# Performance work log

Hardware: AMD Instinct MI355X
Metric: run time of the kernel (lower is better)

Reference implementation:

```python
import jax, jax.numpy as jnp
import numpy as np

B, C, S = 32, 64, 112
RATIO = 8
EPS = 1e-5


def conv1x1(x, w, b):
    # 1x1 conv == channel-mixing matmul. x:[B,C,H,W], w:[O,C], b:[O]
    return jnp.einsum('oc,bchw->bohw', w, x) + b[None, :, None, None]


def dwconv(x, w, b):
    # grouped 1x1 conv with groups=C: per-channel scale + bias
    return x * w[None, :, None, None] + b[None, :, None, None]


def bn(x, g, b):
    # BatchNorm2d in training mode: batch stats over (N,H,W), biased var
    m = x.mean((0, 2, 3), keepdims=True)
    v = x.var((0, 2, 3), keepdims=True)
    return (x - m) * jax.lax.rsqrt(v + EPS) * g[None, :, None, None] + b[None, :, None, None]


def avgpool(x, k):
    # nn.AvgPool2d(k): kernel k, stride k, VALID (floor) padding
    s = jax.lax.reduce_window(x, 0.0, jax.lax.add, (1, 1, k, k), (1, 1, k, k), 'VALID')
    return s / float(k * k)


def setup_inputs() -> dict:
    key = jax.random.key(0)
    ks = jax.random.split(key, 20)
    C2, H = 2 * C, (2 * C) // RATIO

    def n(k, shape, s=0.02):
        return jax.random.normal(k, shape, jnp.float32) * s

    return {
        'rgb': jax.random.normal(ks[0], (B, C, S, S), jnp.float32),
        'fre': jax.random.normal(ks[1], (B, C, S, S), jnp.float32),
        'wq_fad': n(ks[2], (C, C)), 'bq_fad': jnp.zeros((C,), jnp.float32),
        'wq_lfs': n(ks[3], (C, C)), 'bq_lfs': jnp.zeros((C,), jnp.float32),
        'wk_fad': n(ks[4], (C, C)), 'bk_fad': jnp.zeros((C,), jnp.float32),
        'wk_lfs': n(ks[5], (C, C)), 'bk_lfs': jnp.zeros((C,), jnp.float32),
        'fad_gamma': n(ks[6], (1,), 1.0), 'lfs_gamma': n(ks[7], (1,), 1.0),
        'fad_cw': n(ks[8], (C,), 1.0), 'fad_cb': jnp.zeros((C,), jnp.float32),
        'fad_bg': jnp.ones((C,), jnp.float32), 'fad_bb': jnp.zeros((C,), jnp.float32),
        'lfs_cw': n(ks[9], (C,), 1.0), 'lfs_cb': jnp.zeros((C,), jnp.float32),
        'lfs_bg': jnp.ones((C,), jnp.float32), 'lfs_bb': jnp.zeros((C,), jnp.float32),
        'lin1_w': n(ks[10], (3,), 0.3), 'lin2_w': n(ks[11], (3,), 0.3),
        'mlp_w1': n(ks[12], (H, C2)), 'mlp_w2': n(ks[13], (C2, H)),
        'rgb_cw': n(ks[14], (C,), 1.0), 'rgb_cb': jnp.zeros((C,), jnp.float32),
        'rgb_bg': jnp.ones((C,), jnp.float32), 'rgb_bb': jnp.zeros((C,), jnp.float32),
        'fre_cw': n(ks[15], (C,), 1.0), 'fre_cb': jnp.zeros((C,), jnp.float32),
        'fre_bg': jnp.ones((C,), jnp.float32), 'fre_bb': jnp.zeros((C,), jnp.float32),
    }


def reference(rgb, fre, wq_fad, bq_fad, wq_lfs, bq_lfs, wk_fad, bk_fad, wk_lfs, bk_lfs,
              fad_gamma, lfs_gamma, fad_cw, fad_cb, fad_bg, fad_bb,
              lfs_cw, lfs_cb, lfs_bg, lfs_bb, lin1_w, lin2_w, mlp_w1, mlp_w2,
              rgb_cw, rgb_cb, rgb_bg, rgb_bb, fre_cw, fre_cb, fre_bg, fre_bb):
    Bn, Cn, Sz, _ = rgb.shape
    # ---- MixBlock: cross attention over folded (B*C) batch ----
    qF = conv1x1(rgb, wq_fad, bq_fad).reshape(Bn * Cn, Sz, Sz)
    qL = conv1x1(fre, wq_lfs, bq_lfs).reshape(Bn * Cn, Sz, Sz)
    Mq = jnp.concatenate([qF, qL], axis=2)          # [BC, S, 2S]
    kF = conv1x1(rgb, wk_fad, bk_fad).reshape(Bn * Cn, Sz, Sz).transpose(0, 2, 1)
    kL = conv1x1(fre, wk_lfs, bk_lfs).reshape(Bn * Cn, Sz, Sz).transpose(0, 2, 1)
    Mk = jnp.concatenate([kF, kL], axis=1)          # [BC, 2S, S]
    attn = jax.nn.softmax(jnp.matmul(Mq, Mk), axis=-1).reshape(Bn, Cn, Sz, Sz)
    att_lfs = fre * attn * (jax.nn.sigmoid(lfs_gamma) * 2.0 - 1.0)
    y_fad = rgb + bn(dwconv(att_lfs, fad_cw, fad_cb), fad_bg, fad_bb)
    att_fad = rgb * attn * (jax.nn.sigmoid(fad_gamma) * 2.0 - 1.0)
    y_lfs = fre + bn(dwconv(att_fad, lfs_cw, lfs_cb), lfs_bg, lfs_bb)
    # ---- MSCA on concatenated channels ----
    x = jnp.concatenate([y_fad, y_lfs], axis=1)     # [B, 2C, S, S]
    avgs, maxs = [], []
    for k in (3, 5, 7):
        m = avgpool(x, k)
        avgs.append(m.mean((2, 3)))
        maxs.append(m.max((2, 3)))
    a_p = jnp.stack(avgs, -1) @ lin1_w              # [B, 2C]
    m_p = jnp.stack(maxs, -1) @ lin2_w

    def mlp(v):
        h = jax.nn.relu(jnp.einsum('rc,bc->br', mlp_w1, v))
        return jnp.einsum('cr,br->bc', mlp_w2, h)

    ca = jax.nn.sigmoid(mlp(a_p) + mlp(m_p))        # [B, 2C]
    r_c = ca[:, :Cn, None, None]
    f_c = ca[:, Cn:, None, None]
    rgb_out = y_fad + bn(dwconv(r_c * y_fad, rgb_cw, rgb_cb), rgb_bg, rgb_bb)
    fre_out = y_lfs + bn(dwconv(f_c * y_lfs, fre_cw, fre_cb), fre_bg, fre_bb)
    return (rgb_out, fre_out)
```

## Files before the change

### kernel.cpp

```cpp
#include <hip/hip_runtime.h>
#include <hip/hip_bf16.h>
#include <stdint.h>

#define NE 25690112ull
#define PP 12544
#define SS 112
#define EPSV 1e-5f

typedef __attribute__((ext_vector_type(8))) short short8v;
typedef __attribute__((ext_vector_type(4))) float float4v;

__device__ __forceinline__ unsigned short f2bf(float x){
  union { float f; uint32_t u; } v; v.f = x;
  uint32_t r = (v.u + 0x7fffu + ((v.u >> 16) & 1u)) >> 16;
  return (unsigned short)r;
}
__device__ __forceinline__ float bf2f(unsigned short u){ return __uint_as_float(((uint32_t)u) << 16); }

__global__ __launch_bounds__(256) void k1_conv(
    const float* __restrict__ rgb, const float* __restrict__ fre,
    const float* __restrict__ wq_fad, const float* __restrict__ bq_fad,
    const float* __restrict__ wk_fad, const float* __restrict__ bk_fad,
    const float* __restrict__ wq_lfs, const float* __restrict__ bq_lfs,
    const float* __restrict__ wk_lfs, const float* __restrict__ bk_lfs,
    unsigned short* __restrict__ qF, unsigned short* __restrict__ kF,
    unsigned short* __restrict__ qL, unsigned short* __restrict__ kL,
    unsigned short* __restrict__ rgbb, unsigned short* __restrict__ freb)
{
  const int bx = blockIdx.x, b = blockIdx.y, z = blockIdx.z;
  const float* X  = z ? fre : rgb;
  const float* Wq = z ? wq_lfs : wq_fad;
  const float* Bq = z ? bq_lfs : bq_fad;
  const float* Wk = z ? wk_lfs : wk_fad;
  const float* Bk = z ? bk_lfs : bk_fad;
  unsigned short* Oq = z ? qL : qF;
  unsigned short* Ok = z ? kL : kF;
  unsigned short* Xb = z ? freb : rgbb;

  __shared__ __align__(16) unsigned short xs[64 * 260];

  const int tid = threadIdx.x, lane = tid & 63, w = tid >> 6;
  const int lc = lane & 15, l4 = lane >> 4;

  const int p0 = bx*256;
  const size_t xbase = (size_t)b * 64 * PP;
  #pragma unroll
  for (int i = 0; i < 16; ++i){
    const int c = w*16 + i;
    const size_t gof = xbase + (size_t)c*PP + p0 + lane*4;
    float4 xv = *(const float4*)(X + gof);
    ushort4 s;
    s.x = f2bf(xv.x); s.y = f2bf(xv.y); s.z = f2bf(xv.z); s.w = f2bf(xv.w);
    *(ushort4*)(Xb + gof) = s;
    *(ushort4*)(&xs[c*260 + lane*4]) = s;
  }
  __syncthreads();

  short8v afr[4][2];
  #pragma unroll
  for (int t = 0; t < 4; ++t){
    const int p = (t*4 + w)*16 + lc;
    #pragma unroll
    for (int ks = 0; ks < 2; ++ks){
      short8v a;
      #pragma unroll
      for (int j = 0; j < 8; ++j)
        a[j] = (short)xs[(ks*32 + l4*8 + j)*260 + p];
      afr[t][ks] = a;
    }
  }
  __syncthreads();

  #pragma unroll
  for (int arr = 0; arr < 2; ++arr){
    const float* W = arr ? Wk : Wq;
    const float* Bi = arr ? Bk : Bq;
    unsigned short* O = arr ? Ok : Oq;
    short8v wf[4][2];
    float bias[4];
    #pragma unroll
    for (int ot = 0; ot < 4; ++ot){
      bias[ot] = Bi[ot*16 + lc];
      #pragma unroll
      for (int ks = 0; ks < 2; ++ks){
        const int base = (ot*16 + lc)*64 + ks*32 + l4*8;
        const float4 q0 = *(const float4*)(W + base);
        const float4 q1 = *(const float4*)(W + base + 4);
        short8v v;
        v[0]=(short)f2bf(q0.x); v[1]=(short)f2bf(q0.y); v[2]=(short)f2bf(q0.z); v[3]=(short)f2bf(q0.w);
        v[4]=(short)f2bf(q1.x); v[5]=(short)f2bf(q1.y); v[6]=(short)f2bf(q1.z); v[7]=(short)f2bf(q1.w);
        wf[ot][ks] = v;
      }
    }
    #pragma unroll
    for (int t = 0; t < 4; ++t){
      const int pt = (t*4 + w)*16;
      #pragma unroll
      for (int ot = 0; ot < 4; ++ot){
        float4v acc = (float4v){bias[ot], bias[ot], bias[ot], bias[ot]};
        acc = __builtin_amdgcn_mfma_f32_16x16x32_bf16(afr[t][0], wf[ot][0], acc, 0, 0, 0);
        acc = __builtin_amdgcn_mfma_f32_16x16x32_bf16(afr[t][1], wf[ot][1], acc, 0, 0, 0);
        ushort4 u;
        u.x = f2bf(acc[0]); u.y = f2bf(acc[1]); u.z = f2bf(acc[2]); u.w = f2bf(acc[3]);
        const int o = ot*16 + lc;
        uint32_t byteS = (uint32_t)(o*512 + (pt + l4*4)*2) ^ (uint32_t)((o & 7) << 4);
        *(ushort4*)((char*)xs + byteS) = u;
      }
    }
    __syncthreads();
    for (int i = tid; i < 2048; i += 256){
      const int o = i >> 5, s = i & 31;
      uint32_t byteS = (uint32_t)(o*512 + s*16) ^ (uint32_t)((o & 7) << 4);
      short8v v = *(const short8v*)((const char*)xs + byteS);
      *(short8v*)(O + ((size_t)b*64 + o)*PP + p0 + s*8) = v;
    }
    __syncthreads();
  }
}

__global__ __launch_bounds__(448) void k2_attn(
    unsigned short* __restrict__ qF, const unsigned short* __restrict__ qL,
    const unsigned short* __restrict__ kF, const unsigned short* __restrict__ kL,
    const unsigned short* __restrict__ rgbb, const unsigned short* __restrict__ freb,
    const float* __restrict__ fad_gamma, const float* __restrict__ lfs_gamma,
    float* __restrict__ stats)
{
  const int bc = blockIdx.x, c = bc & 63;
  const size_t plane = (size_t)bc * PP;
  __shared__ __align__(16) unsigned short ksF[PP + 16];
  __shared__ __align__(16) unsigned short ksL[PP + 16];
  const int tid = threadIdx.x, lane = tid & 63, w = tid >> 6;
  const int l4 = lane >> 4, lc = lane & 15;

  const unsigned short* qFp = qF + plane;
  const unsigned short* qLp = qL + plane;
  const int qrow = w*16 + lc;
  short8v aF[4], aL[4];
  #pragma unroll
  for (int ks = 0; ks < 4; ++ks){
    const int joff = ks*32 + l4*8;
    if ((ks < 3) || (l4 < 2)){
      aF[ks] = *(const short8v*)(qFp + qrow*SS + joff);
      aL[ks] = *(const short8v*)(qLp + qrow*SS + joff);
    } else {
      aF[ks] = (short8v)(short)0;
      aL[ks] = (short8v)(short)0;
    }
  }

  const uint32_t* kFu = (const uint32_t*)kF + plane/2;
  const uint32_t* kLu = (const uint32_t*)kL + plane/2;
  uint32_t* ksFw = (uint32_t*)ksF;
  uint32_t* ksLw = (uint32_t*)ksL;
  #pragma unroll
  for (int t = 0; t < 14; ++t){
    const int i = tid + t*448;
    ksFw[i] = kFu[i];
    ksLw[i] = kLu[i];
  }
  __syncthreads();

  float4v acc[7];
  #pragma unroll
  for (int ct = 0; ct < 7; ++ct) acc[ct] = (float4v)0.f;
  #pragma unroll
  for (int ks = 0; ks < 4; ++ks){
    #pragma unroll
    for (int ct = 0; ct < 7; ++ct){
      const uint32_t off = (uint32_t)((ct*16 + lc)*224 + ks*64 + l4*16);
      short8v bF = *(const short8v*)((const char*)ksF + off);
      short8v bL = *(const short8v*)((const char*)ksL + off);
      acc[ct] = __builtin_amdgcn_mfma_f32_16x16x32_bf16(aF[ks], bF, acc[ct], 0, 0, 0);
      acc[ct] = __builtin_amdgcn_mfma_f32_16x16x32_bf16(aL[ks], bL, acc[ct], 0, 0, 0);
    }
  }

  ushort4 frv[7], rgv[7];
  #pragma unroll
  for (int t = 0; t < 7; ++t){
    const int i4 = tid + t*448;
    frv[t] = *(const ushort4*)(freb + plane + (size_t)i4*4);
    rgv[t] = *(const ushort4*)(rgbb + plane + (size_t)i4*4);
  }

  const float sF = 2.f/(1.f + __expf(-fad_gamma[0])) - 1.f;
  const float sL = 2.f/(1.f + __expf(-lfs_gamma[0])) - 1.f;
  unsigned short* attnP = qF + plane;
  unsigned short* alin = ksF;

  __syncthreads();
  #pragma unroll
  for (int r = 0; r < 4; ++r){
    const int i = w*16 + l4*4 + r;
    float v[7];
    #pragma unroll
    for (int ct = 0; ct < 7; ++ct) v[ct] = acc[ct][r];
    float m = fmaxf(fmaxf(fmaxf(v[0],v[1]),fmaxf(v[2],v[3])), fmaxf(fmaxf(v[4],v[5]),v[6]));
    #pragma unroll
    for (int off = 8; off; off >>= 1) m = fmaxf(m, __shfl_xor(m, off, 64));
    float e[7]; float s = 0.f;
    #pragma unroll
    for (int ct = 0; ct < 7; ++ct){ e[ct] = __expf(v[ct] - m); s += e[ct]; }
    #pragma unroll
    for (int off = 8; off; off >>= 1) s += __shfl_xor(s, off, 64);
    const float inv = 1.f / s;
    #pragma unroll
    for (int ct = 0; ct < 7; ++ct)
      alin[i*SS + ct*16 + lc] = f2bf(e[ct] * inv);
  }
  __syncthreads();

  float ls1 = 0.f, lq1 = 0.f, ls2 = 0.f, lq2 = 0.f;
  #pragma unroll
  for (int t = 0; t < 7; ++t){
    const int i4 = tid + t*448;
    ushort4 av = *(const ushort4*)(alin + i4*4);
    *(ushort4*)(attnP + (size_t)i4*4) = av;
    const unsigned short* ap = &av.x;
    const unsigned short* fp = &frv[t].x;
    const unsigned short* rp = &rgv[t].x;
    #pragma unroll
    for (int j = 0; j < 4; ++j){
      float a = bf2f(ap[j]);
      float v1 = bf2f(fp[j]) * a * sL;
      float v2 = bf2f(rp[j]) * a * sF;
      ls1 += v1; lq1 += v1*v1; ls2 += v2; lq2 += v2*v2;
    }
  }
  #pragma unroll
  for (int off = 32; off; off >>= 1){
    ls1 += __shfl_xor(ls1, off, 64);
    lq1 += __shfl_xor(lq1, off, 64);
    ls2 += __shfl_xor(ls2, off, 64);
    lq2 += __shfl_xor(lq2, off, 64);
  }
  if (lane == 0){
    atomicAdd(&stats[c],       ls1);
    atomicAdd(&stats[64 + c],  lq1);
    atomicAdd(&stats[128 + c], ls2);
    atomicAdd(&stats[192 + c], lq2);
  }
}

__global__ void k3_affine1(const float* __restrict__ stats,
    const float* __restrict__ fad_cw, const float* __restrict__ fad_bg, const float* __restrict__ fad_bb,
    const float* __restrict__ lfs_cw, const float* __restrict__ lfs_bg, const float* __restrict__ lfs_bb,
    float* __restrict__ AB)
{
  int c = threadIdx.x;
  if (c >= 64) return;
  const float n = 401408.f;
  {
    float m1 = stats[c]/n, v1 = stats[64+c]/n - (stats[c]/n)*(stats[c]/n);
    float cw = fad_cw[c], g = fad_bg[c];
    float rs = rsqrtf(cw*cw*v1 + EPSV);
    AB[c]      = cw*rs*g;
    AB[64 + c] = -cw*m1*rs*g + fad_bb[c];
  }
  {
    float m2 = stats[128+c]/n, v2 = stats[192+c]/n - (stats[128+c]/n)*(stats[128+c]/n);
    float cw = lfs_cw[c], g = lfs_bg[c];
    float rs = rsqrtf(cw*cw*v2 + EPSV);
    AB[128 + c] = cw*rs*g;
    AB[192 + c] = -cw*m2*rs*g + lfs_bb[c];
  }
}

__global__ __launch_bounds__(512) void k4_fuse(
    const unsigned short* __restrict__ attn,
    const unsigned short* __restrict__ rgbb, const unsigned short* __restrict__ freb,
    const float* __restrict__ AB1,
    const float* __restrict__ fad_gamma, const float* __restrict__ lfs_gamma,
    unsigned short* __restrict__ ybf, unsigned short* __restrict__ ybl,
    float* __restrict__ avgstat, float* __restrict__ maxstat,
    float4* __restrict__ planeStats)
{
  const int bc = blockIdx.x, b = bc >> 6, c = bc & 63;
  const size_t plane = (size_t)bc * PP;
  __shared__ unsigned short ys[2][112][113];
  __shared__ float redA[8][4];
  __shared__ float redS[8], redM[8];
  const int tid = threadIdx.x, lane = tid & 63, w = tid >> 6;
  const float sF = 2.f/(1.f + __expf(-fad_gamma[0])) - 1.f;
  const float sL = 2.f/(1.f + __expf(-lfs_gamma[0])) - 1.f;
  const float A1 = AB1[c], B1 = AB1[64+c], A2 = AB1[128+c], B2 = AB1[192+c];
  float s0 = 0.f, q0 = 0.f, s1 = 0.f, q1 = 0.f;

  for (int i4 = tid; i4 < 3136; i4 += 512){
    ushort4 av = *(const ushort4*)(attn + plane + (size_t)i4*4);
    ushort4 rg = *(const ushort4*)(rgbb + plane + (size_t)i4*4);
    ushort4 fr = *(const ushort4*)(freb + plane + (size_t)i4*4);
    float aa[4] = {bf2f(av.x), bf2f(av.y), bf2f(av.z), bf2f(av.w)};
    float rr[4] = {bf2f(rg.x), bf2f(rg.y), bf2f(rg.z), bf2f(rg.w)};
    float ff[4] = {bf2f(fr.x), bf2f(fr.y), bf2f(fr.z), bf2f(fr.w)};
    float y0[4], y1[4];
    ushort4 o0, o1;
    unsigned short* p0 = &o0.x; unsigned short* p1 = &o1.x;
    #pragma unroll
    for (int j = 0; j < 4; ++j){
      float t1 = ff[j]*aa[j]*sL;
      float t2 = rr[j]*aa[j]*sF;
      y0[j] = rr[j] + A1*t1 + B1;
      y1[j] = ff[j] + A2*t2 + B2;
      s0 += y0[j]; q0 += y0[j]*y0[j];
      s1 += y1[j]; q1 += y1[j]*y1[j];
      p0[j] = f2bf(y0[j]);
      p1[j] = f2bf(y1[j]);
    }
    *(ushort4*)(ybf + plane + (size_t)i4*4) = o0;
    *(ushort4*)(ybl + plane + (size_t)i4*4) = o1;
    int r = i4 / 28, c0 = (i4 % 28) * 4;
    #pragma unroll
    for (int j = 0; j < 4; ++j){
      ys[0][r][c0+j] = p0[j];
      ys[1][r][c0+j] = p1[j];
    }
  }
  #pragma unroll
  for (int off = 32; off; off >>= 1){
    s0 += __shfl_xor(s0, off, 64); q0 += __shfl_xor(q0, off, 64);
    s1 += __shfl_xor(s1, off, 64); q1 += __shfl_xor(q1, off, 64);
  }
  if (lane == 0){ redA[w][0] = s0; redA[w][1] = q0; redA[w][2] = s1; redA[w][3] = q1; }
  __syncthreads();
  if (tid == 0){
    float a0=0,a1=0,a2=0,a3=0;
    for (int i = 0; i < 8; ++i){ a0+=redA[i][0]; a1+=redA[i][1]; a2+=redA[i][2]; a3+=redA[i][3]; }
    float4 ps = {a0,a1,a2,a3};
    planeStats[bc] = ps;
  }
  __syncthreads();

  const int kk[3] = {3,5,7};
  const int gg[3] = {37,22,16};
  for (int pl = 0; pl < 2; ++pl){
    const int cc = pl*64 + c;
    for (int ki = 0; ki < 3; ++ki){
      const int k = kk[ki], g = gg[ki];
      float sumAll = 0.f, mx = -3.0e38f;
      for (int win = tid; win < g*g; win += 512){
        int wy = win / g, wx = win % g;
        float s = 0.f;
        for (int dy = 0; dy < k; ++dy)
          for (int dx = 0; dx < k; ++dx)
            s += bf2f(ys[pl][wy*k+dy][wx*k+dx]);
        sumAll += s; mx = fmaxf(mx, s);
      }
      #pragma unroll
      for (int off = 32; off; off >>= 1){
        sumAll += __shfl_xor(sumAll, off, 64);
        mx = fmaxf(mx, __shfl_xor(mx, off, 64));
      }
      if (lane == 0){ redS[w] = sumAll; redM[w] = mx; }
      __syncthreads();
      if (tid == 0){
        float st = 0.f, mt = -3.0e38f;
        for (int i = 0; i < 8; ++i){ st += redS[i]; mt = fmaxf(mt, redM[i]); }
        int idx = (b*128 + cc)*3 + ki;
        avgstat[idx] = st / (float)(k*k*g*g);
        maxstat[idx] = mt / (float)(k*k);
      }
      __syncthreads();
    }
  }
}

__global__ void k6_mlp(const float* __restrict__ avgstat, const float* __restrict__ maxstat,
    const float* __restrict__ lin1, const float* __restrict__ lin2,
    const float* __restrict__ w1, const float* __restrict__ w2,
    float* __restrict__ ca)
{
  const int b = blockIdx.x, tid = threadIdx.x;
  __shared__ float sa[128], sm[128], hA[16], hM[16];
  int idx = (b*128 + tid)*3;
  sa[tid] = avgstat[idx]*lin1[0] + avgstat[idx+1]*lin1[1] + avgstat[idx+2]*lin1[2];
  sm[tid] = maxstat[idx]*lin2[0] + maxstat[idx+1]*lin2[1] + maxstat[idx+2]*lin2[2];
  __syncthreads();
  if (tid < 16){
    float ha = 0.f, hm = 0.f;
    for (int c2 = 0; c2 < 128; ++c2){
      ha += w1[tid*128 + c2]*sa[c2];
      hm += w1[tid*128 + c2]*sm[c2];
    }
    hA[tid] = fmaxf(ha, 0.f); hM[tid] = fmaxf(hm, 0.f);
  }
  __syncthreads();
  float o = 0.f;
  for (int r = 0; r < 16; ++r) o += w2[tid*16 + r]*(hA[r] + hM[r]);
  ca[b*128 + tid] = 1.f/(1.f + __expf(-o));
}

__global__ void k8_affineF(const float4* __restrict__ planeStats, const float* __restrict__ ca,
    const float* __restrict__ rgb_cw, const float* __restrict__ rgb_bg, const float* __restrict__ rgb_bb,
    const float* __restrict__ fre_cw, const float* __restrict__ fre_bg, const float* __restrict__ fre_bb,
    float* __restrict__ ABF)
{
  int t = threadIdx.x;
  if (t >= 128) return;
  int z = t >> 6, c = t & 63;
  float S = 0.f, Q = 0.f;
  for (int b = 0; b < 32; ++b){
    float4 ps = planeStats[b*64 + c];
    float sc = ca[b*128 + t];
    float sp = z ? ps.z : ps.x;
    float qp = z ? ps.w : ps.y;
    S += sc*sp; Q += sc*sc*qp;
  }
  const float n = 401408.f;
  float m = S/n, v = Q/n - m*m;
  float cw = z ? fre_cw[c] : rgb_cw[c];
  float g  = z ? fre_bg[c] : rgb_bg[c];
  float bb = z ? fre_bb[c] : rgb_bb[c];
  float rs = rsqrtf(cw*cw*v + EPSV);
  ABF[z*128 + c]      = cw*rs*g;
  ABF[z*128 + 64 + c] = -cw*m*rs*g + bb;
}

__global__ __launch_bounds__(256) void k9_out(
    const unsigned short* __restrict__ ybf, const unsigned short* __restrict__ ybl,
    const float* __restrict__ ca, const float* __restrict__ ABF,
    float* __restrict__ out)
{
  const int c = blockIdx.x, b = blockIdx.y, z = blockIdx.z;
  const size_t plane = ((size_t)b*64 + c)*PP;
  const unsigned short* y = z ? ybl : ybf;
  float* o = out + (z ? NE : 0) + plane;
  const float sc = ca[b*128 + z*64 + c];
  const float A = ABF[z*128 + c], Bv = ABF[z*128 + 64 + c];
  const float mul = 1.f + A*sc;
  for (int i8 = threadIdx.x; i8 < 1568; i8 += 256){
    short8v yv = *(const short8v*)(y + plane + (size_t)i8*8);
    float4 o0, o1;
    o0.x = bf2f((unsigned short)yv[0])*mul + Bv;
    o0.y = bf2f((unsigned short)yv[1])*mul + Bv;
    o0.z = bf2f((unsigned short)yv[2])*mul + Bv;
    o0.w = bf2f((unsigned short)yv[3])*mul + Bv;
    o1.x = bf2f((unsigned short)yv[4])*mul + Bv;
    o1.y = bf2f((unsigned short)yv[5])*mul + Bv;
    o1.z = bf2f((unsigned short)yv[6])*mul + Bv;
    o1.w = bf2f((unsigned short)yv[7])*mul + Bv;
    *(float4*)(&o[(size_t)i8*8])     = o0;
    *(float4*)(&o[(size_t)i8*8 + 4]) = o1;
  }
}

extern "C" void kernel_launch(void* const* d_in, const int* in_sizes, int n_in,
                              void* d_out, int out_size, void* d_ws, size_t ws_size,
                              hipStream_t stream)
{
  (void)in_sizes; (void)n_in; (void)out_size; (void)ws_size;
  const float* rgb      = (const float*)d_in[0];
  const float* fre      = (const float*)d_in[1];
  const float* wq_fad   = (const float*)d_in[2];
  const float* bq_fad   = (const float*)d_in[3];
  const float* wq_lfs   = (const float*)d_in[4];
  const float* bq_lfs   = (const float*)d_in[5];
  const float* wk_fad   = (const float*)d_in[6];
  const float* bk_fad   = (const float*)d_in[7];
  const float* wk_lfs   = (const float*)d_in[8];
  const float* bk_lfs   = (const float*)d_in[9];
  const float* fad_gamma= (const float*)d_in[10];
  const float* lfs_gamma= (const float*)d_in[11];
  const float* fad_cw   = (const float*)d_in[12];
  const float* fad_bg   = (const float*)d_in[14];
  const float* fad_bb   = (const float*)d_in[15];
  const float* lfs_cw   = (const float*)d_in[16];
  const float* lfs_bg   = (const float*)d_in[18];
  const float* lfs_bb   = (const float*)d_in[19];
  const float* lin1_w   = (const float*)d_in[20];
  const float* lin2_w   = (const float*)d_in[21];
  const float* mlp_w1   = (const float*)d_in[22];
  const float* mlp_w2   = (const float*)d_in[23];
  const float* rgb_cw   = (const float*)d_in[24];
  const float* rgb_bg   = (const float*)d_in[26];
  const float* rgb_bb   = (const float*)d_in[27];
  const float* fre_cw   = (const float*)d_in[28];
  const float* fre_bg   = (const float*)d_in[30];
  const float* fre_bb   = (const float*)d_in[31];

  char* ws = (char*)d_ws;
  unsigned short* qF = (unsigned short*)(ws);
  unsigned short* qL = (unsigned short*)(ws + 2*NE);
  unsigned short* kF = (unsigned short*)(ws + 4*NE);
  unsigned short* kL = (unsigned short*)(ws + 6*NE);
  float* sbase = (float*)(ws + 8*NE);
  float* stats      = sbase;
  float* AB1        = sbase + 256;
  float* avgstat    = sbase + 512;
  float* maxstat    = sbase + 12800;
  float* ca         = sbase + 25088;
  float* ABF        = sbase + 29184;
  float4* planeStats= (float4*)(sbase + 29440);
  unsigned short* rgbb = (unsigned short*)d_out;
  unsigned short* freb = (unsigned short*)d_out + NE;

  hipMemsetAsync(stats, 0, 256*sizeof(float), stream);

  k1_conv<<<dim3(49,32,2), dim3(256), 0, stream>>>(rgb, fre,
      wq_fad, bq_fad, wk_fad, bk_fad, wq_lfs, bq_lfs, wk_lfs, bk_lfs,
      qF, kF, qL, kL, rgbb, freb);
  k2_attn<<<dim3(2048), dim3(448), 0, stream>>>(qF, qL, kF, kL,
      rgbb, freb, fad_gamma, lfs_gamma, stats);
  k3_affine1<<<dim3(1), dim3(64), 0, stream>>>(stats,
      fad_cw, fad_bg, fad_bb, lfs_cw, lfs_bg, lfs_bb, AB1);
  k4_fuse<<<dim3(2048), dim3(512), 0, stream>>>((const unsigned short*)qF,
      rgbb, freb, AB1, fad_gamma, lfs_gamma, kF, kL, avgstat, maxstat, planeStats);
  k6_mlp<<<dim3(32), dim3(128), 0, stream>>>(avgstat, maxstat,
      lin1_w, lin2_w, mlp_w1, mlp_w2, ca);
  k8_affineF<<<dim3(1), dim3(128), 0, stream>>>(planeStats, ca,
      rgb_cw, rgb_bg, rgb_bb, fre_cw, fre_bg, fre_bb, ABF);
  k9_out<<<dim3(64,32,2), dim3(256), 0, stream>>>(kF, kL, ca, ABF,
      (float*)d_out);
}
```

Before: 399.4 us.

## Make k1_conv persistent over four pixel tiles with register prefetch and LDS weights

The 1x1 conv kernel now processes up to four 256-pixel tiles per block, with the grid cut from 49 to 13 blocks in x. Weights are converted to bf16 once per block into swizzled LDS and reused across tiles, instead of being reloaded from global memory per tile. The next tile's fp32 input is prefetched into registers while the current tile is converted and computed, to overlap global loads with MFMA work. The cost is higher register pressure from the 16 float4 prefetch buffer, fewer blocks in flight, and uneven work in the last block.

```diff
diff --git a/kernel.cpp b/kernel.cpp
--- a/kernel.cpp
+++ b/kernel.cpp
@@ -38,83 +38,115 @@
   unsigned short* Xb = z ? freb : rgbb;
 
   __shared__ __align__(16) unsigned short xs[64 * 260];
+  __shared__ __align__(16) unsigned short wlds[2 * 64 * 64];
 
   const int tid = threadIdx.x, lane = tid & 63, w = tid >> 6;
   const int lc = lane & 15, l4 = lane >> 4;
 
-  const int p0 = bx*256;
+  for (int i = tid; i < 2048; i += 256){
+    const int arr = i >> 10, r = i & 1023;
+    const int o = r >> 4, c4 = r & 15;
+    const float* W = arr ? Wk : Wq;
+    const float4 v = *(const float4*)(W + o*64 + c4*4);
+    ushort4 s;
+    s.x = f2bf(v.x); s.y = f2bf(v.y); s.z = f2bf(v.z); s.w = f2bf(v.w);
+    uint32_t byteS = (uint32_t)(arr*8192 + o*128 + c4*8) ^ (uint32_t)((o & 7) << 4);
+    *(ushort4*)((char*)wlds + byteS) = s;
+  }
+  float biasQ[4], biasK[4];
+  #pragma unroll
+  for (int ot = 0; ot < 4; ++ot){
+    biasQ[ot] = Bq[ot*16 + lc];
+    biasK[ot] = Bk[ot*16 + lc];
+  }
+
+  const int nt = min(4, 49 - bx*4);
   const size_t xbase = (size_t)b * 64 * PP;
-  #pragma unroll
-  for (int i = 0; i < 16; ++i){
-    const int c = w*16 + i;
-    const size_t gof = xbase + (size_t)c*PP + p0 + lane*4;
-    float4 xv = *(const float4*)(X + gof);
-    ushort4 s;
-    s.x = f2bf(xv.x); s.y = f2bf(xv.y); s.z = f2bf(xv.z); s.w = f2bf(xv.w);
-    *(ushort4*)(Xb + gof) = s;
-    *(ushort4*)(&xs[c*260 + lane*4]) = s;
-  }
-  __syncthreads();
-
-  short8v afr[4][2];
-  #pragma unroll
-  for (int t = 0; t < 4; ++t){
-    const int p = (t*4 + w)*16 + lc;
-    #pragma unroll
-    for (int ks = 0; ks < 2; ++ks){
-      short8v a;
+
+  float4 xr[16];
+  {
+    const int p0 = bx*4*256;
+    #pragma unroll
+    for (int i = 0; i < 16; ++i)
+      xr[i] = *(const float4*)(X + xbase + (size_t)(w*16 + i)*PP + p0 + lane*4);
+  }
+  __syncthreads();
+
+  for (int t = 0; t < nt; ++t){
+    const int p0 = (bx*4 + t)*256;
+
+    ushort4 sv[16];
+    #pragma unroll
+    for (int i = 0; i < 16; ++i){
+      sv[i].x = f2bf(xr[i].x); sv[i].y = f2bf(xr[i].y);
+      sv[i].z = f2bf(xr[i].z); sv[i].w = f2bf(xr[i].w);
+    }
+    if (t + 1 < nt){
+      const int p1 = p0 + 256;
       #pragma unroll
-      for (int j = 0; j < 8; ++j)
-        a[j] = (short)xs[(ks*32 + l4*8 + j)*260 + p];
-      afr[t][ks] = a;
-    }
-  }
-  __syncthreads();
-
-  #pragma unroll
-  for (int arr = 0; arr < 2; ++arr){
-    const float* W = arr ? Wk : Wq;
-    const float* Bi = arr ? Bk : Bq;
-    unsigned short* O = arr ? Ok : Oq;
-    short8v wf[4][2];
-    float bias[4];
-    #pragma unroll
-    for (int ot = 0; ot < 4; ++ot){
-      bias[ot] = Bi[ot*16 + lc];
+      for (int i = 0; i < 16; ++i)
+        xr[i] = *(const float4*)(X + xbase + (size_t)(w*16 + i)*PP + p1 + lane*4);
+    }
+    #pragma unroll
+    for (int i = 0; i < 16; ++i){
+      const int c = w*16 + i;
+      *(ushort4*)(Xb + xbase + (size_t)c*PP + p0 + lane*4) = sv[i];
+      *(ushort4*)(&xs[c*260 + lane*4]) = sv[i];
+    }
+    __syncthreads();
+
+    short8v afr[4][2];
+    #pragma unroll
+    for (int st = 0; st < 4; ++st){
+      const int p = (st*4 + w)*16 + lc;
       #pragma unroll
       for (int ks = 0; ks < 2; ++ks){
-        const int base = (ot*16 + lc)*64 + ks*32 + l4*8;
-        const float4 q0 = *(const float4*)(W + base);
-        const float4 q1 = *(const float4*)(W + base + 4);
-        short8v v;
-        v[0]=(short)f2bf(q0.x); v[1]=(short)f2bf(q0.y); v[2]=(short)f2bf(q0.z); v[3]=(short)f2bf(q0.w);
-        v[4]=(short)f2bf(q1.x); v[5]=(short)f2bf(q1.y); v[6]=(short)f2bf(q1.z); v[7]=(short)f2bf(q1.w);
-        wf[ot][ks] = v;
+        short8v a;
+        #pragma unroll
+        for (int j = 0; j < 8; ++j)
+          a[j] = (short)xs[(ks*32 + l4*8 + j)*260 + p];
+        afr[st][ks] = a;
       }
     }
-    #pragma unroll
-    for (int t = 0; t < 4; ++t){
-      const int pt = (t*4 + w)*16;
+    __syncthreads();
+
+    #pragma unroll
+    for (int arr = 0; arr < 2; ++arr){
+      unsigned short* O = arr ? Ok : Oq;
+      const float* bias = arr ? biasK : biasQ;
+      short8v wf[4][2];
       #pragma unroll
-      for (int ot = 0; ot < 4; ++ot){
-        float4v acc = (float4v){bias[ot], bias[ot], bias[ot], bias[ot]};
-        acc = __builtin_amdgcn_mfma_f32_16x16x32_bf16(afr[t][0], wf[ot][0], acc, 0, 0, 0);
-        acc = __builtin_amdgcn_mfma_f32_16x16x32_bf16(afr[t][1], wf[ot][1], acc, 0, 0, 0);
-        ushort4 u;
-        u.x = f2bf(acc[0]); u.y = f2bf(acc[1]); u.z = f2bf(acc[2]); u.w = f2bf(acc[3]);
-        const int o = ot*16 + lc;
-        uint32_t byteS = (uint32_t)(o*512 + (pt + l4*4)*2) ^ (uint32_t)((o & 7) << 4);
-        *(ushort4*)((char*)xs + byteS) = u;
+      for (int ot = 0; ot < 4; ++ot)
+        #pragma unroll
+        for (int ks = 0; ks < 2; ++ks){
+          uint32_t byteS = (uint32_t)(arr*8192 + (ot*16 + lc)*128 + ks*64 + l4*16)
+                         ^ (uint32_t)((lc & 7) << 4);
+          wf[ot][ks] = *(const short8v*)((const char*)wlds + byteS);
+        }
+      #pragma unroll
+      for (int st = 0; st < 4; ++st){
+        const int pt = (st*4 + w)*16;
+        #pragma unroll
+        for (int ot = 0; ot < 4; ++ot){
+          float4v acc = (float4v){bias[ot], bias[ot], bias[ot], bias[ot]};
+          acc = __builtin_amdgcn_mfma_f32_16x16x32_bf16(afr[st][0], wf[ot][0], acc, 0, 0, 0);
+          acc = __builtin_amdgcn_mfma_f32_16x16x32_bf16(afr[st][1], wf[ot][1], acc, 0, 0, 0);
+          ushort4 u;
+          u.x = f2bf(acc[0]); u.y = f2bf(acc[1]); u.z = f2bf(acc[2]); u.w = f2bf(acc[3]);
+          const int o = ot*16 + lc;
+          uint32_t byteS = (uint32_t)(o*512 + (pt + l4*4)*2) ^ (uint32_t)((o & 7) << 4);
+          *(ushort4*)((char*)xs + byteS) = u;
+        }
       }
-    }
-    __syncthreads();
-    for (int i = tid; i < 2048; i += 256){
-      const int o = i >> 5, s = i & 31;
-      uint32_t byteS = (uint32_t)(o*512 + s*16) ^ (uint32_t)((o & 7) << 4);
-      short8v v = *(const short8v*)((const char*)xs + byteS);
-      *(short8v*)(O + ((size_t)b*64 + o)*PP + p0 + s*8) = v;
-    }
-    __syncthreads();
+      __syncthreads();
+      for (int i = tid; i < 2048; i += 256){
+        const int o = i >> 5, s = i & 31;
+        uint32_t byteS = (uint32_t)(o*512 + s*16) ^ (uint32_t)((o & 7) << 4);
+        short8v v = *(const short8v*)((const char*)xs + byteS);
+        *(short8v*)(O + ((size_t)b*64 + o)*PP + p0 + s*8) = v;
+      }
+      __syncthreads();
+    }
   }
 }
 
@@ -496,7 +528,7 @@
 
   hipMemsetAsync(stats, 0, 256*sizeof(float), stream);
 
-  k1_conv<<<dim3(49,32,2), dim3(256), 0, stream>>>(rgb, fre,
+  k1_conv<<<dim3(13,32,2), dim3(256), 0, stream>>>(rgb, fre,
       wq_fad, bq_fad, wk_fad, bk_fad, wq_lfs, bq_lfs, wk_lfs, bk_lfs,
       qF, kF, qL, kL, rgbb, freb);
   k2_attn<<<dim3(2048), dim3(448), 0, stream>>>(qF, qL, kF, kL,
```

New measurement: 404.1 us. Within noise of the previous version (+1.2%).

## Recompute y in output kernel from fp32 inputs instead of storing bf16 intermediates

Applied to the files above, without the earlier changes.

Drops the bf16 copies of rgb/fre written by the conv kernel and the bf16 y_fad/y_lfs written by the fuse kernel. The attention, fuse and output kernels now read the original fp32 inputs, and the output kernel recomputes y from attn, the inputs and the first BN affine before applying the final affine. This removes several intermediate writes and reads, but it re-reads the larger fp32 inputs three times, so total traffic may rise.

```diff
diff --git a/kernel.cpp b/kernel.cpp
--- a/kernel.cpp
+++ b/kernel.cpp
@@ -24,8 +24,7 @@
     const float* __restrict__ wq_lfs, const float* __restrict__ bq_lfs,
     const float* __restrict__ wk_lfs, const float* __restrict__ bk_lfs,
     unsigned short* __restrict__ qF, unsigned short* __restrict__ kF,
-    unsigned short* __restrict__ qL, unsigned short* __restrict__ kL,
-    unsigned short* __restrict__ rgbb, unsigned short* __restrict__ freb)
+    unsigned short* __restrict__ qL, unsigned short* __restrict__ kL)
 {
   const int bx = blockIdx.x, b = blockIdx.y, z = blockIdx.z;
   const float* X  = z ? fre : rgb;
@@ -35,7 +34,6 @@
   const float* Bk = z ? bk_lfs : bk_fad;
   unsigned short* Oq = z ? qL : qF;
   unsigned short* Ok = z ? kL : kF;
-  unsigned short* Xb = z ? freb : rgbb;
 
   __shared__ __align__(16) unsigned short xs[64 * 260];
 
@@ -51,7 +49,6 @@
     float4 xv = *(const float4*)(X + gof);
     ushort4 s;
     s.x = f2bf(xv.x); s.y = f2bf(xv.y); s.z = f2bf(xv.z); s.w = f2bf(xv.w);
-    *(ushort4*)(Xb + gof) = s;
     *(ushort4*)(&xs[c*260 + lane*4]) = s;
   }
   __syncthreads();
@@ -121,7 +118,7 @@
 __global__ __launch_bounds__(448) void k2_attn(
     unsigned short* __restrict__ qF, const unsigned short* __restrict__ qL,
     const unsigned short* __restrict__ kF, const unsigned short* __restrict__ kL,
-    const unsigned short* __restrict__ rgbb, const unsigned short* __restrict__ freb,
+    const float* __restrict__ rgb, const float* __restrict__ fre,
     const float* __restrict__ fad_gamma, const float* __restrict__ lfs_gamma,
     float* __restrict__ stats)
 {
@@ -175,14 +172,6 @@
     }
   }
 
-  ushort4 frv[7], rgv[7];
-  #pragma unroll
-  for (int t = 0; t < 7; ++t){
-    const int i4 = tid + t*448;
-    frv[t] = *(const ushort4*)(freb + plane + (size_t)i4*4);
-    rgv[t] = *(const ushort4*)(rgbb + plane + (size_t)i4*4);
-  }
-
   const float sF = 2.f/(1.f + __expf(-fad_gamma[0])) - 1.f;
   const float sL = 2.f/(1.f + __expf(-lfs_gamma[0])) - 1.f;
   unsigned short* attnP = qF + plane;
@@ -216,14 +205,16 @@
     const int i4 = tid + t*448;
     ushort4 av = *(const ushort4*)(alin + i4*4);
     *(ushort4*)(attnP + (size_t)i4*4) = av;
+    float4 fr = *(const float4*)(fre + plane + (size_t)i4*4);
+    float4 rg = *(const float4*)(rgb + plane + (size_t)i4*4);
     const unsigned short* ap = &av.x;
-    const unsigned short* fp = &frv[t].x;
-    const unsigned short* rp = &rgv[t].x;
+    const float fp[4] = {fr.x, fr.y, fr.z, fr.w};
+    const float rp[4] = {rg.x, rg.y, rg.z, rg.w};
     #pragma unroll
     for (int j = 0; j < 4; ++j){
       float a = bf2f(ap[j]);
-      float v1 = bf2f(fp[j]) * a * sL;
-      float v2 = bf2f(rp[j]) * a * sF;
+      float v1 = fp[j] * a * sL;
+      float v2 = rp[j] * a * sF;
       ls1 += v1; lq1 += v1*v1; ls2 += v2; lq2 += v2*v2;
     }
   }
@@ -268,10 +259,9 @@
 
 __global__ __launch_bounds__(512) void k4_fuse(
     const unsigned short* __restrict__ attn,
-    const unsigned short* __restrict__ rgbb, const unsigned short* __restrict__ freb,
+    const float* __restrict__ rgb, const float* __restrict__ fre,
     const float* __restrict__ AB1,
     const float* __restrict__ fad_gamma, const float* __restrict__ lfs_gamma,
-    unsigned short* __restrict__ ybf, unsigned short* __restrict__ ybl,
     float* __restrict__ avgstat, float* __restrict__ maxstat,
     float4* __restrict__ planeStats)
 {
@@ -288,32 +278,22 @@
 
   for (int i4 = tid; i4 < 3136; i4 += 512){
     ushort4 av = *(const ushort4*)(attn + plane + (size_t)i4*4);
-    ushort4 rg = *(const ushort4*)(rgbb + plane + (size_t)i4*4);
-    ushort4 fr = *(const ushort4*)(freb + plane + (size_t)i4*4);
+    float4 rg = *(const float4*)(rgb + plane + (size_t)i4*4);
+    float4 fr = *(const float4*)(fre + plane + (size_t)i4*4);
     float aa[4] = {bf2f(av.x), bf2f(av.y), bf2f(av.z), bf2f(av.w)};
-    float rr[4] = {bf2f(rg.x), bf2f(rg.y), bf2f(rg.z), bf2f(rg.w)};
-    float ff[4] = {bf2f(fr.x), bf2f(fr.y), bf2f(fr.z), bf2f(fr.w)};
-    float y0[4], y1[4];
-    ushort4 o0, o1;
-    unsigned short* p0 = &o0.x; unsigned short* p1 = &o1.x;
+    float rr[4] = {rg.x, rg.y, rg.z, rg.w};
+    float ff[4] = {fr.x, fr.y, fr.z, fr.w};
+    int r = i4 / 28, c0 = (i4 % 28) * 4;
     #pragma unroll
     for (int j = 0; j < 4; ++j){
       float t1 = ff[j]*aa[j]*sL;
       float t2 = rr[j]*aa[j]*sF;
-      y0[j] = rr[j] + A1*t1 + B1;
-      y1[j] = ff[j] + A2*t2 + B2;
-      s0 += y0[j]; q0 += y0[j]*y0[j];
-      s1 += y1[j]; q1 += y1[j]*y1[j];
-      p0[j] = f2bf(y0[j]);
-      p1[j] = f2bf(y1[j]);
-    }
-    *(ushort4*)(ybf + plane + (size_t)i4*4) = o0;
-    *(ushort4*)(ybl + plane + (size_t)i4*4) = o1;
-    int r = i4 / 28, c0 = (i4 % 28) * 4;
-    #pragma unroll
-    for (int j = 0; j < 4; ++j){
-      ys[0][r][c0+j] = p0[j];
-      ys[1][r][c0+j] = p1[j];
+      float y0 = rr[j] + A1*t1 + B1;
+      float y1 = ff[j] + A2*t2 + B2;
+      s0 += y0; q0 += y0*y0;
+      s1 += y1; q1 += y1*y1;
+      ys[0][r][c0+j] = f2bf(y0);
+      ys[1][r][c0+j] = f2bf(y1);
     }
   }
   #pragma unroll
@@ -417,30 +397,43 @@
 }
 
 __global__ __launch_bounds__(256) void k9_out(
-    const unsigned short* __restrict__ ybf, const unsigned short* __restrict__ ybl,
+    const unsigned short* __restrict__ attn,
+    const float* __restrict__ rgb, const float* __restrict__ fre,
+    const float* __restrict__ AB1,
+    const float* __restrict__ fad_gamma, const float* __restrict__ lfs_gamma,
     const float* __restrict__ ca, const float* __restrict__ ABF,
     float* __restrict__ out)
 {
-  const int c = blockIdx.x, b = blockIdx.y, z = blockIdx.z;
+  const int c = blockIdx.x, b = blockIdx.y;
   const size_t plane = ((size_t)b*64 + c)*PP;
-  const unsigned short* y = z ? ybl : ybf;
-  float* o = out + (z ? NE : 0) + plane;
-  const float sc = ca[b*128 + z*64 + c];
-  const float A = ABF[z*128 + c], Bv = ABF[z*128 + 64 + c];
-  const float mul = 1.f + A*sc;
-  for (int i8 = threadIdx.x; i8 < 1568; i8 += 256){
-    short8v yv = *(const short8v*)(y + plane + (size_t)i8*8);
-    float4 o0, o1;
-    o0.x = bf2f((unsigned short)yv[0])*mul + Bv;
-    o0.y = bf2f((unsigned short)yv[1])*mul + Bv;
-    o0.z = bf2f((unsigned short)yv[2])*mul + Bv;
-    o0.w = bf2f((unsigned short)yv[3])*mul + Bv;
-    o1.x = bf2f((unsigned short)yv[4])*mul + Bv;
-    o1.y = bf2f((unsigned short)yv[5])*mul + Bv;
-    o1.z = bf2f((unsigned short)yv[6])*mul + Bv;
-    o1.w = bf2f((unsigned short)yv[7])*mul + Bv;
-    *(float4*)(&o[(size_t)i8*8])     = o0;
-    *(float4*)(&o[(size_t)i8*8 + 4]) = o1;
+  const float sF = 2.f/(1.f + __expf(-fad_gamma[0])) - 1.f;
+  const float sL = 2.f/(1.f + __expf(-lfs_gamma[0])) - 1.f;
+  const float A1 = AB1[c], B1 = AB1[64+c], A2 = AB1[128+c], B2 = AB1[192+c];
+  const float r_c = ca[b*128 + c], f_c = ca[b*128 + 64 + c];
+  const float mul0 = 1.f + ABF[c]*r_c,        add0 = ABF[64 + c];
+  const float mul1 = 1.f + ABF[128 + c]*f_c,  add1 = ABF[192 + c];
+  float* o0 = out + plane;
+  float* o1 = out + NE + plane;
+  for (int i4 = threadIdx.x; i4 < 3136; i4 += 256){
+    ushort4 av = *(const ushort4*)(attn + plane + (size_t)i4*4);
+    float4 rg = *(const float4*)(rgb + plane + (size_t)i4*4);
+    float4 fr = *(const float4*)(fre + plane + (size_t)i4*4);
+    float aa[4] = {bf2f(av.x), bf2f(av.y), bf2f(av.z), bf2f(av.w)};
+    float rr[4] = {rg.x, rg.y, rg.z, rg.w};
+    float ff[4] = {fr.x, fr.y, fr.z, fr.w};
+    float4 v0, v1;
+    float* p0 = &v0.x; float* p1 = &v1.x;
+    #pragma unroll
+    for (int j = 0; j < 4; ++j){
+      float t1 = ff[j]*aa[j]*sL;
+      float t2 = rr[j]*aa[j]*sF;
+      float y0 = rr[j] + A1*t1 + B1;
+      float y1 = ff[j] + A2*t2 + B2;
+      p0[j] = y0*mul0 + add0;
+      p1[j] = y1*mul1 + add1;
+    }
+    *(float4*)(&o0[(size_t)i4*4]) = v0;
+    *(float4*)(&o1[(size_t)i4*4]) = v1;
   }
 }
 
@@ -491,24 +484,22 @@
   float* ca         = sbase + 25088;
   float* ABF        = sbase + 29184;
   float4* planeStats= (float4*)(sbase + 29440);
-  unsigned short* rgbb = (unsigned short*)d_out;
-  unsigned short* freb = (unsigned short*)d_out + NE;
 
   hipMemsetAsync(stats, 0, 256*sizeof(float), stream);
 
   k1_conv<<<dim3(49,32,2), dim3(256), 0, stream>>>(rgb, fre,
       wq_fad, bq_fad, wk_fad, bk_fad, wq_lfs, bq_lfs, wk_lfs, bk_lfs,
-      qF, kF, qL, kL, rgbb, freb);
+      qF, kF, qL, kL);
   k2_attn<<<dim3(2048), dim3(448), 0, stream>>>(qF, qL, kF, kL,
-      rgbb, freb, fad_gamma, lfs_gamma, stats);
+      rgb, fre, fad_gamma, lfs_gamma, stats);
   k3_affine1<<<dim3(1), dim3(64), 0, stream>>>(stats,
       fad_cw, fad_bg, fad_bb, lfs_cw, lfs_bg, lfs_bb, AB1);
   k4_fuse<<<dim3(2048), dim3(512), 0, stream>>>((const unsigned short*)qF,
-      rgbb, freb, AB1, fad_gamma, lfs_gamma, kF, kL, avgstat, maxstat, planeStats);
+      rgb, fre, AB1, fad_gamma, lfs_gamma, avgstat, maxstat, planeStats);
   k6_mlp<<<dim3(32), dim3(128), 0, stream>>>(avgstat, maxstat,
       lin1_w, lin2_w, mlp_w1, mlp_w2, ca);
   k8_affineF<<<dim3(1), dim3(128), 0, stream>>>(planeStats, ca,
       rgb_cw, rgb_bg, rgb_bb, fre_cw, fre_bg, fre_bb, ABF);
-  k9_out<<<dim3(64,32,2), dim3(256), 0, stream>>>(kF, kL, ca, ABF,
-      (float*)d_out);
-}
+  k9_out<<<dim3(64,32), dim3(256), 0, stream>>>((const unsigned short*)qF,
+      rgb, fre, AB1, fad_gamma, lfs_gamma, ca, ABF, (float*)d_out);
+}
```

Result: no change. 401.3 us (+0.5%).
